# Performance work log

Measured on AMD Instinct MI355X. Metric: run time of the kernel, lower is better.

## Reference

```python
import jax, jax.numpy as jnp
import numpy as np

HEADS = 4
HEAD_DIM = 32
SCALE = HEAD_DIM ** (-0.5)


def setup_inputs() -> dict:
    key = jax.random.key(0)
    k1, k2, k3, k4 = jax.random.split(key, 4)
    x = jax.random.normal(k1, (32, 256, 64, 64), dtype=jnp.float32)
    # to_qkv: Conv2d(256 -> 3*heads*head_dim=384, kernel 1x1, bias=False)
    w_qkv = jax.random.normal(k2, (384, 256), dtype=jnp.float32) * 0.02
    # to_out: Conv2d(128 -> 256, kernel 1x1, bias=True)
    w_out = jax.random.normal(k3, (256, 128), dtype=jnp.float32) * 0.02
    b_out = jax.random.normal(k4, (256,), dtype=jnp.float32) * 0.02
    return {"x": x, "w_qkv": w_qkv, "w_out": w_out, "b_out": b_out}


def reference(x, w_qkv, w_out, b_out):
    b, c, H, W = x.shape
    n = H * W
    # 1x1 conv == channel matmul; produce (b, 3, heads, head_dim, n)
    qkv = jnp.einsum('oc,bchw->bohw', w_qkv, x).reshape(b, 3, HEADS, HEAD_DIM, n)
    q, k, v = qkv[:, 0], qkv[:, 1], qkv[:, 2]  # each (b, h, d, n)
    q = jax.nn.softmax(q, axis=-1) * SCALE     # softmax over spatial n
    k = jax.nn.softmax(k, axis=-2)             # softmax over channel d
    # context: (b, h, e, d) -- reduce over n
    context = jnp.einsum('bhen,bhdn->bhed', k, v)
    # out: (b, h, d, n)
    out = jnp.einsum('bhed,bhen->bhdn', context, q)
    out = out.reshape(b, HEADS * HEAD_DIM, H, W)
    # to_out 1x1 conv with bias
    return jnp.einsum('oc,bchw->bohw', w_out, out) + b_out[None, :, None, None]
```

## Files before the change

kernel.cpp:

```cpp
#include <hip/hip_runtime.h>
#include <hip/hip_bf16.h>

#define NTOK 4096
#define SCALE 0.17677669529663687f

#define SWZ(r) ((((r) >> 1) ^ ((r) >> 3)) & 3)

using f32x4 = __attribute__((ext_vector_type(4))) float;
using s16x8 = __attribute__((ext_vector_type(8))) short;

__device__ __forceinline__ ushort bf_rne(float f) {
  unsigned int u = __builtin_bit_cast(unsigned int, f);
  u += 0x7FFFu + ((u >> 16) & 1u);
  return (ushort)(u >> 16);
}
__device__ __forceinline__ void gl_lds16(const ushort* g, ushort* l) {
  __builtin_amdgcn_global_load_lds(
      (const __attribute__((address_space(1))) unsigned int*)g,
      (__attribute__((address_space(3))) unsigned int*)l, 16, 0, 0);
}

__global__ __launch_bounds__(256) void k_cvt_w(const float* __restrict__ w,
                                               ushort* __restrict__ wb) {
  const int i = blockIdx.x * 256 + threadIdx.x;
  const float4 v = reinterpret_cast<const float4*>(w)[i];
  ushort4 h;
  h.x = bf_rne(v.x); h.y = bf_rne(v.y); h.z = bf_rne(v.z); h.w = bf_rne(v.w);
  reinterpret_cast<ushort4*>(wb)[i] = h;
}

__global__ __launch_bounds__(256) void k_cvt_x(const float* __restrict__ x,
                                               ushort* __restrict__ xT) {
  const int n0 = blockIdx.x * 64;
  const int c0 = blockIdx.y * 128;
  const int b  = blockIdx.z;
  __shared__ ushort T[64 * 136];
  const int t = threadIdx.x;
  const int rr = t >> 4;
  const int nq = t & 15;
  const float* xp = x + ((size_t)b * 256 + c0) * NTOK + n0;
#pragma unroll
  for (int p = 0; p < 8; ++p) {
    const int c = p * 16 + rr;
    const float4 v = *reinterpret_cast<const float4*>(xp + (size_t)c * NTOK + nq * 4);
    T[(nq * 4 + 0) * 136 + c] = bf_rne(v.x);
    T[(nq * 4 + 1) * 136 + c] = bf_rne(v.y);
    T[(nq * 4 + 2) * 136 + c] = bf_rne(v.z);
    T[(nq * 4 + 3) * 136 + c] = bf_rne(v.w);
  }
  __syncthreads();
  ushort* op = xT + ((size_t)b * NTOK + n0) * 256 + c0;
#pragma unroll
  for (int i = 0; i < 4; ++i) {
    const int row = i * 16 + rr;
    *reinterpret_cast<uint4*>(op + (size_t)row * 256 + nq * 8) =
        *reinterpret_cast<const uint4*>(&T[row * 136 + nq * 8]);
  }
}

__global__ __launch_bounds__(256) void k_qkv_mfma(const ushort* __restrict__ xT,
                                                  const ushort* __restrict__ wb,
                                                  ushort* __restrict__ Ecn,
                                                  ushort* __restrict__ kb,
                                                  ushort* __restrict__ vb,
                                                  float* __restrict__ spart) {
  const int n0 = blockIdx.x * 128;
  const int o0 = blockIdx.y * 128;
  const int b  = blockIdx.z;
  const ushort* xTb = xT + (size_t)b * NTOK * 256;

  __shared__ ushort As[2 * 4096];
  __shared__ ushort Bs[2 * 4096];

  const int t = threadIdx.x;
  const int lane = t & 63;
  const int wv = t >> 6;
  const int wr = wv >> 1, wc = wv & 1;
  const int lm = lane & 15;
  const int lk = lane >> 4;

  int aoff[4], boff[4];
#pragma unroll
  for (int mf = 0; mf < 4; ++mf) {
    const int ar = wr * 64 + mf * 16 + lm;
    aoff[mf] = ar * 32 + 8 * (lk ^ SWZ(ar));
  }
#pragma unroll
  for (int nf = 0; nf < 4; ++nf) {
    const int br = wc * 64 + nf * 16 + lm;
    boff[nf] = br * 32 + 8 * (lk ^ SWZ(br));
  }
  const int s1 = t, s2 = t + 256;
  const int r1 = s1 >> 2, q1 = (s1 & 3) ^ SWZ(r1);
  const int r2 = s2 >> 2, q2 = (s2 & 3) ^ SWZ(r2);
  const size_t ga1 = (size_t)(o0 + r1) * 256 + q1 * 8;
  const size_t ga2 = (size_t)(o0 + r2) * 256 + q2 * 8;
  const size_t gb1 = (size_t)(n0 + r1) * 256 + q1 * 8;
  const size_t gb2 = (size_t)(n0 + r2) * 256 + q2 * 8;
  const int lbase1 = wv * 512;
  const int lbase2 = 2048 + wv * 512;

  f32x4 acc[4][4];
#pragma unroll
  for (int i = 0; i < 4; ++i)
#pragma unroll
    for (int j = 0; j < 4; ++j) acc[i][j] = (f32x4){0.f, 0.f, 0.f, 0.f};

  gl_lds16(wb + ga1, As + lbase1);
  gl_lds16(wb + ga2, As + lbase2);
  gl_lds16(xTb + gb1, Bs + lbase1);
  gl_lds16(xTb + gb2, Bs + lbase2);
  __syncthreads();

  for (int it = 0; it < 8; ++it) {
    const int cb = (it & 1) * 4096;
    if (it < 7) {
      const int nb = ((it + 1) & 1) * 4096;
      const size_t c1 = (size_t)(it + 1) * 32;
      gl_lds16(wb + ga1 + c1, As + nb + lbase1);
      gl_lds16(wb + ga2 + c1, As + nb + lbase2);
      gl_lds16(xTb + gb1 + c1, Bs + nb + lbase1);
      gl_lds16(xTb + gb2 + c1, Bs + nb + lbase2);
    }
    s16x8 af[4], bf[4];
#pragma unroll
    for (int mf = 0; mf < 4; ++mf)
      af[mf] = *reinterpret_cast<const s16x8*>(As + cb + aoff[mf]);
#pragma unroll
    for (int nf = 0; nf < 4; ++nf)
      bf[nf] = *reinterpret_cast<const s16x8*>(Bs + cb + boff[nf]);
#pragma unroll
    for (int mf = 0; mf < 4; ++mf)
#pragma unroll
      for (int nf = 0; nf < 4; ++nf)
        acc[mf][nf] = __builtin_amdgcn_mfma_f32_16x16x32_bf16(af[mf], bf[nf], acc[mf][nf], 0, 0, 0);
    __syncthreads();
  }

  if (blockIdx.y == 0) {
    ushort* C = Ecn + (size_t)b * 128 * NTOK + n0;
    float* sp = spart + (((size_t)b * 32 + blockIdx.x) * 2 + wc) * 128;
#pragma unroll
    for (int mf = 0; mf < 4; ++mf) {
#pragma unroll
      for (int r = 0; r < 4; ++r) {
        const int ch = wr * 64 + mf * 16 + lk * 4 + r;
        float s = 0.f;
#pragma unroll
        for (int nf = 0; nf < 4; ++nf) {
          const float e = __expf(acc[mf][nf][r]);
          s += e;
          C[(size_t)ch * NTOK + wc * 64 + nf * 16 + lm] = bf_rne(e);
        }
        s += __shfl_xor(s, 1, 64);
        s += __shfl_xor(s, 2, 64);
        s += __shfl_xor(s, 4, 64);
        s += __shfl_xor(s, 8, 64);
        if (lm == 0) sp[ch] = s;
      }
    }
  } else if (blockIdx.y == 1) {
#pragma unroll
    for (int nf = 0; nf < 4; ++nf) {
#pragma unroll
      for (int g = 0; g < 2; ++g) {
        float m = -1e30f;
#pragma unroll
        for (int mm = 0; mm < 2; ++mm)
#pragma unroll
          for (int r = 0; r < 4; ++r)
            m = fmaxf(m, acc[g * 2 + mm][nf][r]);
        m = fmaxf(m, __shfl_xor(m, 16, 64));
        m = fmaxf(m, __shfl_xor(m, 32, 64));
        float s = 0.f;
#pragma unroll
        for (int mm = 0; mm < 2; ++mm)
#pragma unroll
          for (int r = 0; r < 4; ++r) {
            const float e = __expf(acc[g * 2 + mm][nf][r] - m);
            acc[g * 2 + mm][nf][r] = e;
            s += e;
          }
        s += __shfl_xor(s, 16, 64);
        s += __shfl_xor(s, 32, 64);
        const float inv = 1.0f / s;
#pragma unroll
        for (int mm = 0; mm < 2; ++mm)
#pragma unroll
          for (int r = 0; r < 4; ++r) acc[g * 2 + mm][nf][r] *= inv;
      }
    }
    ushort* C = kb + (size_t)b * 128 * NTOK + n0;
#pragma unroll
    for (int mf = 0; mf < 4; ++mf) {
      const int row0 = wr * 64 + mf * 16 + lk * 4;
#pragma unroll
      for (int nf = 0; nf < 4; ++nf) {
        const int col = wc * 64 + nf * 16 + lm;
#pragma unroll
        for (int r = 0; r < 4; ++r)
          C[(size_t)(row0 + r) * NTOK + col] = bf_rne(acc[mf][nf][r]);
      }
    }
  } else {
    ushort* C = vb + (size_t)b * 128 * NTOK + n0;
#pragma unroll
    for (int mf = 0; mf < 4; ++mf) {
      const int row0 = wr * 64 + mf * 16 + lk * 4;
#pragma unroll
      for (int nf = 0; nf < 4; ++nf) {
        const int col = wc * 64 + nf * 16 + lm;
#pragma unroll
        for (int r = 0; r < 4; ++r)
          C[(size_t)(row0 + r) * NTOK + col] = bf_rne(acc[mf][nf][r]);
      }
    }
  }
}

__global__ __launch_bounds__(256) void k_context_mfma(const ushort* __restrict__ kb,
                                                      const ushort* __restrict__ vb,
                                                      float* __restrict__ ctx_part) {
  const int bh = blockIdx.x;
  const int w = threadIdx.x >> 6;
  const int lane = threadIdx.x & 63;
  const int lm = lane & 15, lk = lane >> 4;
  const ushort* kp = kb + (size_t)bh * 32 * NTOK + (size_t)w * 1024;
  const ushort* vp = vb + (size_t)bh * 32 * NTOK + (size_t)w * 1024;
  f32x4 acc[2][2];
#pragma unroll
  for (int i = 0; i < 2; ++i)
#pragma unroll
    for (int j = 0; j < 2; ++j) acc[i][j] = (f32x4){0.f, 0.f, 0.f, 0.f};
#pragma unroll 4
  for (int ks = 0; ks < 32; ++ks) {
    const int coff = ks * 32 + lk * 8;
    const s16x8 a0 = *reinterpret_cast<const s16x8*>(kp + (size_t)lm * NTOK + coff);
    const s16x8 a1 = *reinterpret_cast<const s16x8*>(kp + (size_t)(16 + lm) * NTOK + coff);
    const s16x8 b0 = *reinterpret_cast<const s16x8*>(vp + (size_t)lm * NTOK + coff);
    const s16x8 b1 = *reinterpret_cast<const s16x8*>(vp + (size_t)(16 + lm) * NTOK + coff);
    acc[0][0] = __builtin_amdgcn_mfma_f32_16x16x32_bf16(a0, b0, acc[0][0], 0, 0, 0);
    acc[0][1] = __builtin_amdgcn_mfma_f32_16x16x32_bf16(a0, b1, acc[0][1], 0, 0, 0);
    acc[1][0] = __builtin_amdgcn_mfma_f32_16x16x32_bf16(a1, b0, acc[1][0], 0, 0, 0);
    acc[1][1] = __builtin_amdgcn_mfma_f32_16x16x32_bf16(a1, b1, acc[1][1], 0, 0, 0);
  }
  float* op = ctx_part + ((size_t)bh * 4 + w) * 1024;
#pragma unroll
  for (int et = 0; et < 2; ++et)
#pragma unroll
    for (int dt = 0; dt < 2; ++dt)
#pragma unroll
      for (int r = 0; r < 4; ++r)
        op[(et * 16 + lk * 4 + r) * 32 + dt * 16 + lm] = acc[et][dt][r];
}

__global__ __launch_bounds__(256) void k_w2(const float* __restrict__ ctx_part,
                                            const float* __restrict__ spart,
                                            const float* __restrict__ w_out,
                                            ushort* __restrict__ W2b) {
  const int b = blockIdx.x;
  const int t = threadIdx.x;
  __shared__ float ctx[4096];
  __shared__ float fbuf[128];
#pragma unroll
  for (int i = 0; i < 16; ++i) {
    const int idx = t + 256 * i;
    const int h = idx >> 10, ed = idx & 1023;
    const float* cp = ctx_part + ((size_t)((b * 4 + h) * 4)) * 1024 + ed;
    ctx[idx] = cp[0] + cp[1024] + cp[2048] + cp[3072];
  }
  if (t < 128) {
    float s = 0.f;
    for (int p = 0; p < 64; ++p) s += spart[((size_t)b * 64 + p) * 128 + t];
    fbuf[t] = SCALE / s;
  }
  __syncthreads();
  const float* wrow = w_out + (size_t)t * 128;
  ushort* wout_row = W2b + ((size_t)b * 256 + t) * 128;
  float wv[32];
  for (int h = 0; h < 4; ++h) {
#pragma unroll
    for (int d = 0; d < 32; ++d) wv[d] = wrow[h * 32 + d];
#pragma unroll 4
    for (int e = 0; e < 32; ++e) {
      float a = 0.f;
#pragma unroll
      for (int d = 0; d < 32; ++d) a += wv[d] * ctx[h * 1024 + e * 32 + d];
      wout_row[h * 32 + e] = bf_rne(a * fbuf[h * 32 + e]);
    }
  }
}

__global__ __launch_bounds__(256) void k_out_mfma(const ushort* __restrict__ Ecn,
                                                  const ushort* __restrict__ W2b,
                                                  const float* __restrict__ b_out,
                                                  float* __restrict__ out) {
  const int n0 = blockIdx.x * 128;
  const int o0 = blockIdx.y * 128;
  const int b  = blockIdx.z;
  const ushort* A  = W2b + (size_t)b * 256 * 128;
  const ushort* Bq = Ecn + (size_t)b * 128 * NTOK;

  __shared__ ushort As[8192];
  __shared__ ushort Bt[8192];

  const int t = threadIdx.x;
  const int lane = t & 63;
  const int wv = t >> 6;
  const int wr = wv >> 1, wc = wv & 1;
  const int lm = lane & 15;
  const int lk = lane >> 4;

  int aoff[4][2], boff[4][2];
#pragma unroll
  for (int mf = 0; mf < 4; ++mf) {
    const int ar = wr * 64 + mf * 16 + lm;
#pragma unroll
    for (int ks = 0; ks < 2; ++ks)
      aoff[mf][ks] = ar * 64 + 8 * ((ks * 4 + lk) ^ (ar & 7));
  }
#pragma unroll
  for (int nf = 0; nf < 4; ++nf) {
    const int br = wc * 64 + nf * 16 + lm;
#pragma unroll
    for (int ks = 0; ks < 2; ++ks)
      boff[nf][ks] = br * 64 + 8 * ((ks * 4 + lk) ^ (br & 7));
  }
  size_t gaA[4];
  int lb[4];
#pragma unroll
  for (int i = 0; i < 4; ++i) {
    const int s_total = t + 256 * i;
    const int r = s_total >> 3;
    const int q = (s_total & 7) ^ (r & 7);
    gaA[i] = (size_t)(o0 + r) * 128 + q * 8;
    lb[i] = wv * 512 + i * 2048;
  }
  int bst[8], bn[8], bcg[8];
#pragma unroll
  for (int i = 0; i < 8; ++i) {
    const int u = t + 256 * i;
    bn[i] = u & 127;
    bcg[i] = u >> 7;
    bst[i] = bn[i] * 64 + 8 * ((bcg[i] >> 1) ^ (bn[i] & 7)) + (bcg[i] & 1) * 4;
  }

  f32x4 acc[4][4];
#pragma unroll
  for (int i = 0; i < 4; ++i)
#pragma unroll
    for (int j = 0; j < 4; ++j) acc[i][j] = (f32x4){0.f, 0.f, 0.f, 0.f};

  for (int it = 0; it < 2; ++it) {
    const size_t c0 = (size_t)it * 64;
    __syncthreads();
#pragma unroll
    for (int i = 0; i < 4; ++i)
      gl_lds16(A + gaA[i] + c0, As + lb[i]);
#pragma unroll
    for (int i = 0; i < 8; ++i) {
      const ushort* gp = Bq + (c0 + bcg[i] * 4) * NTOK + n0 + bn[i];
      ushort4 hvec;
      hvec.x = gp[0];
      hvec.y = gp[NTOK];
      hvec.z = gp[2 * NTOK];
      hvec.w = gp[3 * NTOK];
      *reinterpret_cast<ushort4*>(Bt + bst[i]) = hvec;
    }
    __syncthreads();
#pragma unroll
    for (int ks = 0; ks < 2; ++ks) {
      s16x8 af[4], bf[4];
#pragma unroll
      for (int mf = 0; mf < 4; ++mf)
        af[mf] = *reinterpret_cast<const s16x8*>(As + aoff[mf][ks]);
#pragma unroll
      for (int nf = 0; nf < 4; ++nf)
        bf[nf] = *reinterpret_cast<const s16x8*>(Bt + boff[nf][ks]);
#pragma unroll
      for (int mf = 0; mf < 4; ++mf)
#pragma unroll
        for (int nf = 0; nf < 4; ++nf)
          acc[mf][nf] = __builtin_amdgcn_mfma_f32_16x16x32_bf16(af[mf], bf[nf], acc[mf][nf], 0, 0, 0);
    }
  }

  float* C = out + ((size_t)b * 256 + o0) * NTOK + n0;
#pragma unroll
  for (int mf = 0; mf < 4; ++mf) {
    const int row0 = wr * 64 + mf * 16 + lk * 4;
#pragma unroll
    for (int nf = 0; nf < 4; ++nf) {
      const int col = wc * 64 + nf * 16 + lm;
#pragma unroll
      for (int r = 0; r < 4; ++r) {
        const float bias = b_out[o0 + row0 + r];
        C[(size_t)(row0 + r) * NTOK + col] = acc[mf][nf][r] + bias;
      }
    }
  }
}

extern "C" void kernel_launch(void* const* d_in, const int* in_sizes, int n_in,
                              void* d_out, int out_size, void* d_ws, size_t ws_size,
                              hipStream_t stream) {
  const float* x     = (const float*)d_in[0];
  const float* w_qkv = (const float*)d_in[1];
  const float* w_out = (const float*)d_in[2];
  const float* b_out = (const float*)d_in[3];
  float* out = (float*)d_out;

  ushort* xT  = (ushort*)d_ws;
  ushort* kb  = xT + (size_t)33554432;
  ushort* vb  = kb + (size_t)16777216;
  ushort* Ecn = vb + (size_t)16777216;
  float*  ctx_part = (float*)(Ecn + (size_t)16777216);
  float*  spart    = ctx_part + 524288;
  ushort* wb  = (ushort*)(spart + 262144);
  ushort* W2b = wb + 98304;

  k_cvt_w<<<96, 256, 0, stream>>>(w_qkv, wb);
  k_cvt_x<<<dim3(64, 2, 32), 256, 0, stream>>>(x, xT);
  k_qkv_mfma<<<dim3(32, 3, 32), 256, 0, stream>>>(xT, wb, Ecn, kb, vb, spart);
  k_context_mfma<<<128, 256, 0, stream>>>(kb, vb, ctx_part);
  k_w2<<<32, 256, 0, stream>>>(ctx_part, spart, w_out, W2b);
  k_out_mfma<<<dim3(32, 2, 32), 256, 0, stream>>>(Ecn, W2b, b_out, out);
}
```

Baseline: 195.3 us.

## Fuse fp32-to-bf16 transpose of x into the QKV GEMM loader

Removes the separate k_cvt_x kernel that wrote a transposed bf16 copy of x. The QKV GEMM now reads fp32 x directly with register prefetch, converts it to bf16 and stores it swizzled into LDS, cutting one full read and write of a 64MB-class intermediate. In exchange the LDS buffers become single-buffered and need an extra barrier per iteration. Because blockIdx.y spans 3 output tiles, x is now re-read and re-converted three times, and the fp32 loads are strided scalar accesses.

After: 176.6 us. -9.6%, faster.

```diff
diff --git a/kernel.cpp b/kernel.cpp
--- a/kernel.cpp
+++ b/kernel.cpp
@@ -13,6 +13,12 @@
   unsigned int u = __builtin_bit_cast(unsigned int, f);
   u += 0x7FFFu + ((u >> 16) & 1u);
   return (ushort)(u >> 16);
+}
+__device__ __forceinline__ unsigned int pk2(float a, float b) {
+  __hip_bfloat162 h = __float22bfloat162_rn(make_float2(a, b));
+  unsigned int u;
+  __builtin_memcpy(&u, &h, 4);
+  return u;
 }
 __device__ __forceinline__ void gl_lds16(const ushort* g, ushort* l) {
   __builtin_amdgcn_global_load_lds(
@@ -29,36 +35,7 @@
   reinterpret_cast<ushort4*>(wb)[i] = h;
 }
 
-__global__ __launch_bounds__(256) void k_cvt_x(const float* __restrict__ x,
-                                               ushort* __restrict__ xT) {
-  const int n0 = blockIdx.x * 64;
-  const int c0 = blockIdx.y * 128;
-  const int b  = blockIdx.z;
-  __shared__ ushort T[64 * 136];
-  const int t = threadIdx.x;
-  const int rr = t >> 4;
-  const int nq = t & 15;
-  const float* xp = x + ((size_t)b * 256 + c0) * NTOK + n0;
-#pragma unroll
-  for (int p = 0; p < 8; ++p) {
-    const int c = p * 16 + rr;
-    const float4 v = *reinterpret_cast<const float4*>(xp + (size_t)c * NTOK + nq * 4);
-    T[(nq * 4 + 0) * 136 + c] = bf_rne(v.x);
-    T[(nq * 4 + 1) * 136 + c] = bf_rne(v.y);
-    T[(nq * 4 + 2) * 136 + c] = bf_rne(v.z);
-    T[(nq * 4 + 3) * 136 + c] = bf_rne(v.w);
-  }
-  __syncthreads();
-  ushort* op = xT + ((size_t)b * NTOK + n0) * 256 + c0;
-#pragma unroll
-  for (int i = 0; i < 4; ++i) {
-    const int row = i * 16 + rr;
-    *reinterpret_cast<uint4*>(op + (size_t)row * 256 + nq * 8) =
-        *reinterpret_cast<const uint4*>(&T[row * 136 + nq * 8]);
-  }
-}
-
-__global__ __launch_bounds__(256) void k_qkv_mfma(const ushort* __restrict__ xT,
+__global__ __launch_bounds__(256) void k_qkv_mfma(const float* __restrict__ x,
                                                   const ushort* __restrict__ wb,
                                                   ushort* __restrict__ Ecn,
                                                   ushort* __restrict__ kb,
@@ -67,10 +44,10 @@
   const int n0 = blockIdx.x * 128;
   const int o0 = blockIdx.y * 128;
   const int b  = blockIdx.z;
-  const ushort* xTb = xT + (size_t)b * NTOK * 256;
-
-  __shared__ ushort As[2 * 4096];
-  __shared__ ushort Bs[2 * 4096];
+  const float* xb = x + (size_t)b * 256 * NTOK;
+
+  __shared__ ushort As[4096];
+  __shared__ ushort Bs[4096];
 
   const int t = threadIdx.x;
   const int lane = t & 63;
@@ -95,10 +72,16 @@
   const int r2 = s2 >> 2, q2 = (s2 & 3) ^ SWZ(r2);
   const size_t ga1 = (size_t)(o0 + r1) * 256 + q1 * 8;
   const size_t ga2 = (size_t)(o0 + r2) * 256 + q2 * 8;
-  const size_t gb1 = (size_t)(n0 + r1) * 256 + q1 * 8;
-  const size_t gb2 = (size_t)(n0 + r2) * 256 + q2 * 8;
   const int lbase1 = wv * 512;
   const int lbase2 = 2048 + wv * 512;
+  int sst[2], sn[2], sco[2];
+#pragma unroll
+  for (int i = 0; i < 2; ++i) {
+    const int u = t + 256 * i;
+    sn[i] = u & 127;
+    sco[i] = u >> 7;
+    sst[i] = sn[i] * 32 + 8 * (sco[i] ^ SWZ(sn[i]));
+  }
 
   f32x4 acc[4][4];
 #pragma unroll
@@ -106,29 +89,42 @@
 #pragma unroll
     for (int j = 0; j < 4; ++j) acc[i][j] = (f32x4){0.f, 0.f, 0.f, 0.f};
 
-  gl_lds16(wb + ga1, As + lbase1);
-  gl_lds16(wb + ga2, As + lbase2);
-  gl_lds16(xTb + gb1, Bs + lbase1);
-  gl_lds16(xTb + gb2, Bs + lbase2);
-  __syncthreads();
+  float pre[16];
+#pragma unroll
+  for (int i = 0; i < 2; ++i)
+#pragma unroll
+    for (int j = 0; j < 8; ++j)
+      pre[i * 8 + j] = xb[(size_t)(sco[i] * 8 + j) * NTOK + n0 + sn[i]];
 
   for (int it = 0; it < 8; ++it) {
-    const int cb = (it & 1) * 4096;
+    const size_t c0 = (size_t)it * 32;
+    gl_lds16(wb + ga1 + c0, As + lbase1);
+    gl_lds16(wb + ga2 + c0, As + lbase2);
+#pragma unroll
+    for (int i = 0; i < 2; ++i) {
+      union { s16x8 v; unsigned int u[4]; } pk;
+      pk.u[0] = pk2(pre[i * 8 + 0], pre[i * 8 + 1]);
+      pk.u[1] = pk2(pre[i * 8 + 2], pre[i * 8 + 3]);
+      pk.u[2] = pk2(pre[i * 8 + 4], pre[i * 8 + 5]);
+      pk.u[3] = pk2(pre[i * 8 + 6], pre[i * 8 + 7]);
+      *reinterpret_cast<s16x8*>(Bs + sst[i]) = pk.v;
+    }
+    __syncthreads();
     if (it < 7) {
-      const int nb = ((it + 1) & 1) * 4096;
-      const size_t c1 = (size_t)(it + 1) * 32;
-      gl_lds16(wb + ga1 + c1, As + nb + lbase1);
-      gl_lds16(wb + ga2 + c1, As + nb + lbase2);
-      gl_lds16(xTb + gb1 + c1, Bs + nb + lbase1);
-      gl_lds16(xTb + gb2 + c1, Bs + nb + lbase2);
+      const size_t c1 = c0 + 32;
+#pragma unroll
+      for (int i = 0; i < 2; ++i)
+#pragma unroll
+        for (int j = 0; j < 8; ++j)
+          pre[i * 8 + j] = xb[(c1 + sco[i] * 8 + j) * NTOK + n0 + sn[i]];
     }
     s16x8 af[4], bf[4];
 #pragma unroll
     for (int mf = 0; mf < 4; ++mf)
-      af[mf] = *reinterpret_cast<const s16x8*>(As + cb + aoff[mf]);
+      af[mf] = *reinterpret_cast<const s16x8*>(As + aoff[mf]);
 #pragma unroll
     for (int nf = 0; nf < 4; ++nf)
-      bf[nf] = *reinterpret_cast<const s16x8*>(Bs + cb + boff[nf]);
+      bf[nf] = *reinterpret_cast<const s16x8*>(Bs + boff[nf]);
 #pragma unroll
     for (int mf = 0; mf < 4; ++mf)
 #pragma unroll
@@ -410,8 +406,7 @@
   const float* b_out = (const float*)d_in[3];
   float* out = (float*)d_out;
 
-  ushort* xT  = (ushort*)d_ws;
-  ushort* kb  = xT + (size_t)33554432;
+  ushort* kb  = (ushort*)d_ws;
   ushort* vb  = kb + (size_t)16777216;
   ushort* Ecn = vb + (size_t)16777216;
   float*  ctx_part = (float*)(Ecn + (size_t)16777216);
@@ -420,8 +415,7 @@
   ushort* W2b = wb + 98304;
 
   k_cvt_w<<<96, 256, 0, stream>>>(w_qkv, wb);
-  k_cvt_x<<<dim3(64, 2, 32), 256, 0, stream>>>(x, xT);
-  k_qkv_mfma<<<dim3(32, 3, 32), 256, 0, stream>>>(xT, wb, Ecn, kb, vb, spart);
+  k_qkv_mfma<<<dim3(32, 3, 32), 256, 0, stream>>>(x, wb, Ecn, kb, vb, spart);
   k_context_mfma<<<128, 256, 0, stream>>>(kb, vb, ctx_part);
   k_w2<<<32, 256, 0, stream>>>(ctx_part, spart, w_out, W2b);
   k_out_mfma<<<dim3(32, 2, 32), 256, 0, stream>>>(Ecn, W2b, b_out, out);
```
